# Kernel optimization log

Measured on AMD Instinct MI355X. Metric: run time of the kernel, lower is better.

Reference implementation:

```python
import jax, jax.numpy as jnp
import numpy as np

NUM_HEADS = 12


def setup_inputs() -> dict:
    key = jax.random.key(0)
    k_x, k_m, k_qkv, k_proj = jax.random.split(key, 4)
    B, N, C = 2, 2048, 768
    x = jax.random.normal(k_x, (B, N, C), dtype=jnp.float32)
    # binary key mask: 1 = attend, 0 = masked out
    mask = jax.random.randint(k_m, (B, N), 0, 2).astype(jnp.int32)
    # torch Linear(dim, dim*3, bias=False): stored here as [in, out]
    w_qkv = jax.random.normal(k_qkv, (C, 3 * C), dtype=jnp.float32) * 0.02
    w_proj = jax.random.normal(k_proj, (C, C), dtype=jnp.float32) * 0.02
    b_proj = jnp.zeros((C,), dtype=jnp.float32)
    return {"x": x, "mask": mask, "w_qkv": w_qkv, "w_proj": w_proj, "b_proj": b_proj}


def reference(x, mask, w_qkv, w_proj, b_proj):
    B, N, C = x.shape
    H = NUM_HEADS
    hd = C // H
    scale = hd ** -0.5
    qkv = (x @ w_qkv).reshape(B, N, 3, H, hd)
    q, k, v = jnp.moveaxis(qkv, 2, 0)            # each [B, N, H, hd]
    attn = jnp.einsum('bnhd,bmhd->bhnm', q, k) * scale  # [B, H, N, N]
    # faithful masked_softmax: unstable exp (no max subtraction), mask keys, renormalize
    m = mask.astype(x.dtype)[:, None, None, :]   # [B, 1, 1, N]
    x_exp = jnp.exp(attn) * m
    attn = x_exp / x_exp.sum(-1, keepdims=True)
    out = jnp.einsum('bhnm,bmhd->bnhd', attn, v).reshape(B, N, C)
    return out @ w_proj + b_proj
```

## Files before the change

kernel.cpp:

```cpp
#include <hip/hip_runtime.h>
#include <cstdint>

#define NB 2
#define NSEQ 2048
#define CDIM 768
#define NH 12
#define HD 64
#define NTOK (NB*NSEQ)
#define QKV_COLS (3*CDIM)
#define NBLK ((NSEQ/64)*NH*NB)

typedef short bf16x8 __attribute__((ext_vector_type(8)));
typedef short bf16x4 __attribute__((ext_vector_type(4)));
typedef float f32x4  __attribute__((ext_vector_type(4)));
typedef short short4v __attribute__((ext_vector_type(4)));
typedef unsigned int uint4v __attribute__((ext_vector_type(4)));

#define MFMA16(a,b,c) __builtin_amdgcn_mfma_f32_16x16x32_bf16(a,b,c,0,0,0)

__device__ __forceinline__ short f2b(float f) {
    uint32_t u = __builtin_bit_cast(uint32_t, f);
    u += 0x7fffu + ((u >> 16) & 1u);
    return (short)(u >> 16);
}
__device__ __forceinline__ float b2f(short s) {
    return __builtin_bit_cast(float, (uint32_t)((uint32_t)(unsigned short)s << 16));
}
__device__ __forceinline__ unsigned pack2(float a, float b) {
    unsigned ua = __builtin_bit_cast(unsigned, a) + 0x7fffu;
    unsigned ub = __builtin_bit_cast(unsigned, b) + 0x7fffu;
    return __builtin_amdgcn_perm(ub, ua, 0x07060302u);
}
__device__ __forceinline__ float fexp2(float x) {
#if __has_builtin(__builtin_amdgcn_exp2f)
    return __builtin_amdgcn_exp2f(x);
#else
    return __expf(x * 0.69314718055994531f);
#endif
}
__device__ __forceinline__ void gll16(const short* g, short* l) {
    __builtin_amdgcn_global_load_lds(
        (const __attribute__((address_space(1))) unsigned int*)g,
        (__attribute__((address_space(3))) unsigned int*)l, 16, 0, 0);
}

__global__ __launch_bounds__(256) void prep_kernel(
    const float* __restrict__ x, const float* __restrict__ w_qkv,
    const float* __restrict__ w_proj, const int* __restrict__ mask,
    short* __restrict__ xb, short* __restrict__ wqt, short* __restrict__ wpt,
    short* __restrict__ maskb)
{
    __shared__ float tile[32][33];
    const int bid = blockIdx.x, t = threadIdx.x;
    if (bid < 3072) {
        int i = bid * 256 + t;
        float4 v = ((const float4*)x)[i];
        short4v o = { f2b(v.x), f2b(v.y), f2b(v.z), f2b(v.w) };
        ((short4v*)xb)[i] = o;
        return;
    }
    if (bid >= 5376) {
        int i = ((bid - 5376) << 11) + (t << 3);
        int4 a = *(const int4*)(mask + i);
        int4 c = *(const int4*)(mask + i + 4);
        const short NEG = (short)0xC680;
        short4v o0 = { a.x ? (short)0 : NEG, a.y ? (short)0 : NEG,
                       a.z ? (short)0 : NEG, a.w ? (short)0 : NEG };
        short4v o1 = { c.x ? (short)0 : NEG, c.y ? (short)0 : NEG,
                       c.z ? (short)0 : NEG, c.w ? (short)0 : NEG };
        *(short4v*)(maskb + i) = o0;
        *(short4v*)(maskb + i + 4) = o1;
        return;
    }
    const float* w; short* wt; int K, NC, n0, k0;
    if (bid < 3072 + 1728) {
        int r = bid - 3072;
        w = w_qkv; wt = wqt; K = CDIM; NC = QKV_COLS;
        n0 = (r % 72) * 32; k0 = (r / 72) * 32;
    } else {
        int r = bid - 4800;
        w = w_proj; wt = wpt; K = CDIM; NC = CDIM;
        n0 = (r % 24) * 32; k0 = (r / 24) * 32;
    }
    #pragma unroll
    for (int i = 0; i < 4; ++i) {
        int idx = t + i * 256; int r = idx >> 5, c = idx & 31;
        tile[r][c] = w[(size_t)(k0 + r) * NC + n0 + c];
    }
    __syncthreads();
    #pragma unroll
    for (int i = 0; i < 4; ++i) {
        int idx = t + i * 256; int r = idx >> 5, c = idx & 31;
        wt[(size_t)(n0 + r) * K + k0 + c] = f2b(tile[c][r]);
    }
}

__global__ __launch_bounds__(256) void gemm_qkv(
    const short* __restrict__ A ,
    const short* __restrict__ B ,
    short* __restrict__ qb, short* __restrict__ kb, short* __restrict__ vt)
{
    __shared__ short As[128 * 32];
    __shared__ short Bs[128 * 32];
    const int t = threadIdx.x;
    const int lane = t & 63, wid = t >> 6;
    const int quad = lane >> 4, l16 = lane & 15;
    const int wA = wid >> 1, wB = wid & 1;
    const int n0 = blockIdx.x * 128;
    const int m0 = blockIdx.y * 128;

    const int srow = wid * 16 + (lane >> 2), schunk = (lane & 3) * 8;
    const short* ag0 = A + (size_t)(n0 + srow) * CDIM + schunk;
    const short* ag1 = ag0 + (size_t)64 * CDIM;
    const short* bg0 = B + (size_t)(m0 + srow) * CDIM + schunk;
    const short* bg1 = bg0 + (size_t)64 * CDIM;
    short* asl0 = &As[(wid * 16) * 32];
    short* asl1 = &As[(wid * 16 + 64) * 32];
    short* bsl0 = &Bs[(wid * 16) * 32];
    short* bsl1 = &Bs[(wid * 16 + 64) * 32];

    f32x4 acc[4][4] = {};
    for (int k0 = 0; k0 < CDIM; k0 += 32) {
        __syncthreads();
        gll16(ag0 + k0, asl0);
        gll16(ag1 + k0, asl1);
        gll16(bg0 + k0, bsl0);
        gll16(bg1 + k0, bsl1);
        __syncthreads();
        bf16x8 af[4], bf[4];
        #pragma unroll
        for (int i = 0; i < 4; ++i)
            af[i] = *(const bf16x8*)&As[(wA*64 + i*16 + l16) * 32 + quad*8];
        #pragma unroll
        for (int j = 0; j < 4; ++j)
            bf[j] = *(const bf16x8*)&Bs[(wB*64 + j*16 + l16) * 32 + quad*8];
        #pragma unroll
        for (int i = 0; i < 4; ++i)
            #pragma unroll
            for (int j = 0; j < 4; ++j)
                acc[i][j] = MFMA16(af[i], bf[j], acc[i][j]);
    }

    const int colbase = n0 + wA * 64;
    const int s = colbase / CDIM;
    const int h = (colbase - s * CDIM) >> 6;
    const int b = m0 >> 11;
    const size_t bh = (size_t)(b * NH + h);
    const float qsc = (s == 0) ? 0.18033688011112042f : 1.0f;
    #pragma unroll
    for (int i = 0; i < 4; ++i) {
        const int d0 = i*16 + quad*4;
        #pragma unroll
        for (int j = 0; j < 4; ++j) {
            int tok = (m0 + wB*64 + j*16 + l16) & (NSEQ - 1);
            if (s < 2) {
                short* dst = (s == 0 ? qb : kb) + (bh * NSEQ + tok) * HD + d0;
                short4v o = { f2b(acc[i][j][0] * qsc), f2b(acc[i][j][1] * qsc),
                              f2b(acc[i][j][2] * qsc), f2b(acc[i][j][3] * qsc) };
                *(short4v*)dst = o;
            } else {
                short* dst = vt + (bh * HD + d0) * NSEQ + tok;
                #pragma unroll
                for (int r = 0; r < 4; ++r)
                    dst[(size_t)r * NSEQ] = f2b(acc[i][j][r]);
            }
        }
    }
}

#define STAGE_K(KT, BUF) do {                                                    \
    short* kb_ = (BUF);                                                          \
    _Pragma("unroll")                                                            \
    for (int j = 0; j < 4; ++j)                                                  \
        gll16(kp + (size_t)((KT) + rK[j]) * HD + cK[j]*8,                        \
              kb_ + wid*2048 + j*512);                                           \
} while (0)

#define STAGE_V(KT) do {                                                         \
    _Pragma("unroll")                                                            \
    for (int j = 0; j < 4; ++j)                                                  \
        gll16(vp + (size_t)dV[j] * NSEQ + (KT) + cV[j]*8,                        \
              Vb + wid*2048 + j*512);                                            \
} while (0)

#define QKBODY(KT, KBUF) do {                                                    \
    const short* KsB_ = (KBUF) + kg*4096;                                        \
    _Pragma("unroll")                                                            \
    for (int ks = 0; ks < 2; ++ks) {                                             \
        short4v mi0_ = *(const short4v*)&Msk[(KT) + kg*64 + ks*16 + qrow4];      \
        short4v mi1_ = *(const short4v*)&Msk[(KT) + kg*64 + 32 + ks*16 + qrow4]; \
        const int kro_ = (ks*16 + l16) * 64;                                     \
        bf16x8 kf00_ = *(const bf16x8*)&KsB_[kro_ + kc0];                        \
        bf16x8 kf01_ = *(const bf16x8*)&KsB_[kro_ + kc1];                        \
        bf16x8 kf10_ = *(const bf16x8*)&KsB_[2048 + kro_ + kc0];                 \
        bf16x8 kf11_ = *(const bf16x8*)&KsB_[2048 + kro_ + kc1];                 \
        f32x4 m0v_ = { b2f(mi0_[0]), b2f(mi0_[1]),                               \
                       b2f(mi0_[2]), b2f(mi0_[3]) };                             \
        f32x4 m1v_ = { b2f(mi1_[0]), b2f(mi1_[1]),                               \
                       b2f(mi1_[2]), b2f(mi1_[3]) };                             \
        _Pragma("unroll")                                                        \
        for (int jq = 0; jq < 2; ++jq) {                                         \
            f32x4 s0_ = m0v_, s1_ = m1v_;                                        \
            s0_ = MFMA16(kf00_, qf[jq][0], s0_);                                 \
            s0_ = MFMA16(kf01_, qf[jq][1], s0_);                                 \
            s1_ = MFMA16(kf10_, qf[jq][0], s1_);                                 \
            s1_ = MFMA16(kf11_, qf[jq][1], s1_);                                 \
            float e0 = fexp2(s0_[0]);                                            \
            float e1 = fexp2(s0_[1]);                                            \
            float e2 = fexp2(s0_[2]);                                            \
            float e3 = fexp2(s0_[3]);                                            \
            float f0 = fexp2(s1_[0]);                                            \
            float f1 = fexp2(s1_[1]);                                            \
            float f2 = fexp2(s1_[2]);                                            \
            float f3 = fexp2(s1_[3]);                                            \
            uint4v pk_ = { pack2(e0, e1), pack2(e2, e3),                         \
                           pack2(f0, f1), pack2(f2, f3) };                       \
            pb[jq][ks] = __builtin_bit_cast(bf16x8, pk_);                        \
        }                                                                        \
    }                                                                            \
} while (0)

#define PVBODY() do {                                                            \
    _Pragma("unroll")                                                            \
    for (int ks = 0; ks < 2; ++ks) {                                             \
        lacc[0] = MFMA16(onesv, pb[0][ks], lacc[0]);                             \
        lacc[1] = MFMA16(onesv, pb[1][ks], lacc[1]);                             \
    }                                                                            \
    _Pragma("unroll")                                                            \
    for (int it = 0; it < 4; ++it) {                                             \
        const int vrow_ = (it*16 + l16) * 128;                                   \
        _Pragma("unroll")                                                        \
        for (int ks = 0; ks < 2; ++ks) {                                         \
            const int gl_ = (((kg*8 + ks*2 + qh) ^ l16) << 3) + vsub;            \
            const int gh_ = (((kg*8 + 4 + ks*2 + qh) ^ l16) << 3) + vsub;        \
            bf16x4 lo_ = *(const bf16x4*)&Vb[vrow_ + gl_];                       \
            bf16x4 hi_ = *(const bf16x4*)&Vb[vrow_ + gh_];                       \
            bf16x8 vf_ = __builtin_shufflevector(lo_, hi_, 0,1,2,3,4,5,6,7);     \
            o_acc[0][it] = MFMA16(vf_, pb[0][ks], o_acc[0][it]);                 \
            o_acc[1][it] = MFMA16(vf_, pb[1][ks], o_acc[1][it]);                 \
        }                                                                        \
    }                                                                            \
} while (0)

#define WAITV_BAR() do {                                                         \
    asm volatile("s_waitcnt vmcnt(4)" ::: "memory");                             \
    __builtin_amdgcn_sched_barrier(0);                                           \
    __builtin_amdgcn_s_barrier();                                                \
} while (0)

#define WAITK_BAR() do {                                                         \
    asm volatile("s_waitcnt vmcnt(0)" ::: "memory");                             \
    __builtin_amdgcn_sched_barrier(0);                                           \
    __builtin_amdgcn_s_barrier();                                                \
} while (0)

__global__ __launch_bounds__(256, 3) void attn_kernel(
    const short* __restrict__ qb, const short* __restrict__ kb,
    const short* __restrict__ vt, const short* __restrict__ maskb,
    short* __restrict__ ao)
{
    __shared__ __align__(16) short Kb[2][8192];
    __shared__ __align__(16) short Vb[8192];
    __shared__ __align__(16) short Msk[2048];

    const int t = threadIdx.x;
    const int lane = t & 63, wid = t >> 6;
    const int quad = lane >> 4, l16 = lane & 15;
    const int qg = wid >> 1, kg = wid & 1;
    const int id = blockIdx.x;
    const int idx = id >> 3;
    const int bh = (id & 7) + ((idx % 3) << 3);
    const int q0 = (idx / 3) << 6;
    const int b = bh / NH, h = bh - b * NH;
    const size_t hoff = (size_t)bh * NSEQ * HD;
    const short* qp = qb + hoff;
    const short* kp = kb + hoff;
    const short* vp = vt + hoff;
    const int qrow4 = quad * 4;

    int rK[4], cK[4], dV[4], cV[4];
    #pragma unroll
    for (int j = 0; j < 4; ++j) {
        int o = wid * 4096 + j * 1024 + lane * 16;
        rK[j] = o >> 7;
        cK[j] = ((o >> 4) & 7) ^ (rK[j] & 7);
        dV[j] = o >> 8;
        cV[j] = ((o >> 4) & 15) ^ (dV[j] & 15);
    }
    const int r7 = l16 & 7;
    const int kc0 = ((quad     ^ r7) << 3);
    const int kc1 = (((quad+4) ^ r7) << 3);
    const int qh = quad >> 1;
    const int vsub = (quad & 1) * 4;

    bf16x8 qf[2][2];
    {
        const short* qr = qp + (size_t)(q0 + qg*32 + l16) * HD + quad*8;
        qf[0][0] = *(const bf16x8*)qr;
        qf[0][1] = *(const bf16x8*)(qr + 32);
        qf[1][0] = *(const bf16x8*)(qr + 16*HD);
        qf[1][1] = *(const bf16x8*)(qr + 16*HD + 32);
    }

    const short one_ = (short)0x3F80;
    const bf16x8 onesv = { one_, one_, one_, one_, one_, one_, one_, one_ };

    f32x4 o_acc[2][4] = {};
    f32x4 lacc[2] = {};
    bf16x8 pb[2][2];

    STAGE_K(0, Kb[0]);
    gll16(maskb + b * NSEQ + t * 8, Msk + wid * 512);
    __syncthreads();

    for (int kt = 0; kt < NSEQ; kt += 256) {
        STAGE_V(kt);
        __builtin_amdgcn_sched_barrier(0);
        STAGE_K(kt + 128, Kb[1]);
        __builtin_amdgcn_sched_barrier(0);
        QKBODY(kt, Kb[0]);
        WAITV_BAR();
        __builtin_amdgcn_s_setprio(1);
        PVBODY();
        __builtin_amdgcn_s_setprio(0);
        WAITK_BAR();

        STAGE_V(kt + 128);
        __builtin_amdgcn_sched_barrier(0);
        STAGE_K((kt + 256) & (NSEQ - 1), Kb[0]);
        __builtin_amdgcn_sched_barrier(0);
        QKBODY(kt + 128, Kb[1]);
        WAITV_BAR();
        __builtin_amdgcn_s_setprio(1);
        PVBODY();
        __builtin_amdgcn_s_setprio(0);
        WAITK_BAR();
    }

    f32x4* red = (f32x4*)Kb;
    const int rbase = (qg*64 + lane) * 9;
    if (kg == 1) {
        #pragma unroll
        for (int jq = 0; jq < 2; ++jq)
            #pragma unroll
            for (int it = 0; it < 4; ++it)
                red[rbase + jq*4 + it] = o_acc[jq][it];
        f32x4 lv = { lacc[0][0], lacc[1][0], 0.f, 0.f };
        red[rbase + 8] = lv;
    }
    __syncthreads();
    if (kg == 0) {
        f32x4 lv = red[rbase + 8];
        const float inv0 = 1.0f / (lacc[0][0] + lv[0]);
        const float inv1 = 1.0f / (lacc[1][0] + lv[1]);
        #pragma unroll
        for (int jq = 0; jq < 2; ++jq) {
            const float inv = jq ? inv1 : inv0;
            const int tok = b * NSEQ + q0 + qg*32 + jq*16 + l16;
            short* dst = ao + (size_t)tok * CDIM + h * HD + qrow4;
            #pragma unroll
            for (int it = 0; it < 4; ++it) {
                f32x4 o_ = o_acc[jq][it];
                f32x4 r_ = red[rbase + jq*4 + it];
                short4v o = { f2b((o_[0] + r_[0]) * inv),
                              f2b((o_[1] + r_[1]) * inv),
                              f2b((o_[2] + r_[2]) * inv),
                              f2b((o_[3] + r_[3]) * inv) };
                *(short4v*)(dst + it*16) = o;
            }
        }
    }
}

__global__ __launch_bounds__(256) void gemm_proj(
    const short* __restrict__ A ,
    const short* __restrict__ B ,
    const float* __restrict__ bias, float* __restrict__ out)
{
    __shared__ short As[128 * 32];
    __shared__ short Bs[128 * 32];
    const int t = threadIdx.x;
    const int lane = t & 63, wid = t >> 6;
    const int quad = lane >> 4, l16 = lane & 15;
    const int wA = wid >> 1, wB = wid & 1;
    const int n0 = blockIdx.x * 128;
    const int m0 = blockIdx.y * 128;

    const int srow = wid * 16 + (lane >> 2), schunk = (lane & 3) * 8;
    const short* ag0 = A + (size_t)(n0 + srow) * CDIM + schunk;
    const short* ag1 = ag0 + (size_t)64 * CDIM;
    const short* bg0 = B + (size_t)(m0 + srow) * CDIM + schunk;
    const short* bg1 = bg0 + (size_t)64 * CDIM;
    short* asl0 = &As[(wid * 16) * 32];
    short* asl1 = &As[(wid * 16 + 64) * 32];
    short* bsl0 = &Bs[(wid * 16) * 32];
    short* bsl1 = &Bs[(wid * 16 + 64) * 32];

    f32x4 acc[4][4] = {};
    for (int k0 = 0; k0 < CDIM; k0 += 32) {
        __syncthreads();
        gll16(ag0 + k0, asl0);
        gll16(ag1 + k0, asl1);
        gll16(bg0 + k0, bsl0);
        gll16(bg1 + k0, bsl1);
        __syncthreads();
        bf16x8 af[4], bf[4];
        #pragma unroll
        for (int i = 0; i < 4; ++i)
            af[i] = *(const bf16x8*)&As[(wA*64 + i*16 + l16) * 32 + quad*8];
        #pragma unroll
        for (int j = 0; j < 4; ++j)
            bf[j] = *(const bf16x8*)&Bs[(wB*64 + j*16 + l16) * 32 + quad*8];
        #pragma unroll
        for (int i = 0; i < 4; ++i)
            #pragma unroll
            for (int j = 0; j < 4; ++j)
                acc[i][j] = MFMA16(af[i], bf[j], acc[i][j]);
    }

    #pragma unroll
    for (int i = 0; i < 4; ++i) {
        int col0 = n0 + wA*64 + i*16 + quad*4;
        float4 bias4 = *(const float4*)&bias[col0];
        #pragma unroll
        for (int j = 0; j < 4; ++j) {
            int tok = m0 + wB*64 + j*16 + l16;
            float4 o = { acc[i][j][0] + bias4.x, acc[i][j][1] + bias4.y,
                         acc[i][j][2] + bias4.z, acc[i][j][3] + bias4.w };
            *(float4*)(out + (size_t)tok * CDIM + col0) = o;
        }
    }
}

extern "C" void kernel_launch(void* const* d_in, const int* in_sizes, int n_in,
                              void* d_out, int out_size, void* d_ws, size_t ws_size,
                              hipStream_t stream)
{
    const float* x      = (const float*)d_in[0];
    const int*   mask   = (const int*)d_in[1];
    const float* w_qkv  = (const float*)d_in[2];
    const float* w_proj = (const float*)d_in[3];
    const float* b_proj = (const float*)d_in[4];
    float* out = (float*)d_out;

    const size_t SZ = (size_t)NTOK * CDIM;
    short* xb  = (short*)d_ws;
    short* wqt = xb  + SZ;
    short* wpt = wqt + (size_t)QKV_COLS * CDIM;
    short* qb  = wpt + (size_t)CDIM * CDIM;
    short* kb  = qb  + SZ;
    short* vt  = kb  + SZ;
    short* ao  = vt  + SZ;
    short* maskb = ao + SZ;

    dim3 blk(256);
    prep_kernel<<<dim3(5378), blk, 0, stream>>>(x, w_qkv, w_proj, mask,
                                                xb, wqt, wpt, maskb);
    gemm_qkv<<<dim3(QKV_COLS/128, NTOK/128), blk, 0, stream>>>(wqt, xb, qb, kb, vt);
    attn_kernel<<<dim3(NBLK), blk, 0, stream>>>(qb, kb, vt, maskb, ao);
    gemm_proj<<<dim3(CDIM/128, NTOK/128), blk, 0, stream>>>(wpt, ao, b_proj, out);
}
```

Baseline: 159.0 us.

## Double-buffer LDS tiles in QKV and projection GEMMs; vectorize weight transpose

Both GEMM kernels now keep two LDS stages: the next K-tile is loaded with direct global-to-LDS loads while MFMAs run on the current one, and there is one barrier per iteration instead of two. The aim is to hide global load latency behind the matrix math. The weight transpose/convert prep kernel now reads float4 and writes short4 per thread instead of scalar loops. LDS use per block doubles, which may lower occupancy. Whether the async LDS writes are ordered correctly depends on the barrier also waiting on the outstanding loads.

```diff
diff --git a/kernel.cpp b/kernel.cpp
--- a/kernel.cpp
+++ b/kernel.cpp
@@ -82,26 +82,34 @@
         w = w_proj; wt = wpt; K = CDIM; NC = CDIM;
         n0 = (r % 24) * 32; k0 = (r / 24) * 32;
     }
-    #pragma unroll
-    for (int i = 0; i < 4; ++i) {
-        int idx = t + i * 256; int r = idx >> 5, c = idx & 31;
-        tile[r][c] = w[(size_t)(k0 + r) * NC + n0 + c];
+    const int r = t >> 3, c4 = (t & 7) * 4;
+    {
+        float4 v = *(const float4*)&w[(size_t)(k0 + r) * NC + n0 + c4];
+        tile[r][c4 + 0] = v.x; tile[r][c4 + 1] = v.y;
+        tile[r][c4 + 2] = v.z; tile[r][c4 + 3] = v.w;
     }
     __syncthreads();
-    #pragma unroll
-    for (int i = 0; i < 4; ++i) {
-        int idx = t + i * 256; int r = idx >> 5, c = idx & 31;
-        wt[(size_t)(n0 + r) * K + k0 + c] = f2b(tile[c][r]);
-    }
-}
+    {
+        short4v o = { f2b(tile[c4 + 0][r]), f2b(tile[c4 + 1][r]),
+                      f2b(tile[c4 + 2][r]), f2b(tile[c4 + 3][r]) };
+        *(short4v*)&wt[(size_t)(n0 + r) * K + k0 + c4] = o;
+    }
+}
+
+#define GSTAGE(K0V, B) do {                                                      \
+    gll16(ag0 + (K0V), As + (B)*4096 + (wid*16)*32);                             \
+    gll16(ag1 + (K0V), As + (B)*4096 + (wid*16 + 64)*32);                        \
+    gll16(bg0 + (K0V), Bs + (B)*4096 + (wid*16)*32);                             \
+    gll16(bg1 + (K0V), Bs + (B)*4096 + (wid*16 + 64)*32);                        \
+} while (0)
 
 __global__ __launch_bounds__(256) void gemm_qkv(
     const short* __restrict__ A ,
     const short* __restrict__ B ,
     short* __restrict__ qb, short* __restrict__ kb, short* __restrict__ vt)
 {
-    __shared__ short As[128 * 32];
-    __shared__ short Bs[128 * 32];
+    __shared__ short As[2 * 4096];
+    __shared__ short Bs[2 * 4096];
     const int t = threadIdx.x;
     const int lane = t & 63, wid = t >> 6;
     const int quad = lane >> 4, l16 = lane & 15;
@@ -114,31 +122,30 @@
     const short* ag1 = ag0 + (size_t)64 * CDIM;
     const short* bg0 = B + (size_t)(m0 + srow) * CDIM + schunk;
     const short* bg1 = bg0 + (size_t)64 * CDIM;
-    short* asl0 = &As[(wid * 16) * 32];
-    short* asl1 = &As[(wid * 16 + 64) * 32];
-    short* bsl0 = &Bs[(wid * 16) * 32];
-    short* bsl1 = &Bs[(wid * 16 + 64) * 32];
 
     f32x4 acc[4][4] = {};
+    GSTAGE(0, 0);
+    __syncthreads();
+    int buf = 0;
     for (int k0 = 0; k0 < CDIM; k0 += 32) {
-        __syncthreads();
-        gll16(ag0 + k0, asl0);
-        gll16(ag1 + k0, asl1);
-        gll16(bg0 + k0, bsl0);
-        gll16(bg1 + k0, bsl1);
-        __syncthreads();
+        if (k0 + 32 < CDIM) GSTAGE(k0 + 32, buf ^ 1);
+        __builtin_amdgcn_sched_barrier(0);
+        const short* As_ = As + buf * 4096;
+        const short* Bs_ = Bs + buf * 4096;
         bf16x8 af[4], bf[4];
         #pragma unroll
         for (int i = 0; i < 4; ++i)
-            af[i] = *(const bf16x8*)&As[(wA*64 + i*16 + l16) * 32 + quad*8];
+            af[i] = *(const bf16x8*)&As_[(wA*64 + i*16 + l16) * 32 + quad*8];
         #pragma unroll
         for (int j = 0; j < 4; ++j)
-            bf[j] = *(const bf16x8*)&Bs[(wB*64 + j*16 + l16) * 32 + quad*8];
+            bf[j] = *(const bf16x8*)&Bs_[(wB*64 + j*16 + l16) * 32 + quad*8];
         #pragma unroll
         for (int i = 0; i < 4; ++i)
             #pragma unroll
             for (int j = 0; j < 4; ++j)
                 acc[i][j] = MFMA16(af[i], bf[j], acc[i][j]);
+        __syncthreads();
+        buf ^= 1;
     }
 
     const int colbase = n0 + wA * 64;
@@ -377,8 +384,8 @@
     const short* __restrict__ B ,
     const float* __restrict__ bias, float* __restrict__ out)
 {
-    __shared__ short As[128 * 32];
-    __shared__ short Bs[128 * 32];
+    __shared__ short As[2 * 4096];
+    __shared__ short Bs[2 * 4096];
     const int t = threadIdx.x;
     const int lane = t & 63, wid = t >> 6;
     const int quad = lane >> 4, l16 = lane & 15;
@@ -391,31 +398,30 @@
     const short* ag1 = ag0 + (size_t)64 * CDIM;
     const short* bg0 = B + (size_t)(m0 + srow) * CDIM + schunk;
     const short* bg1 = bg0 + (size_t)64 * CDIM;
-    short* asl0 = &As[(wid * 16) * 32];
-    short* asl1 = &As[(wid * 16 + 64) * 32];
-    short* bsl0 = &Bs[(wid * 16) * 32];
-    short* bsl1 = &Bs[(wid * 16 + 64) * 32];
 
     f32x4 acc[4][4] = {};
+    GSTAGE(0, 0);
+    __syncthreads();
+    int buf = 0;
     for (int k0 = 0; k0 < CDIM; k0 += 32) {
-        __syncthreads();
-        gll16(ag0 + k0, asl0);
-        gll16(ag1 + k0, asl1);
-        gll16(bg0 + k0, bsl0);
-        gll16(bg1 + k0, bsl1);
-        __syncthreads();
+        if (k0 + 32 < CDIM) GSTAGE(k0 + 32, buf ^ 1);
+        __builtin_amdgcn_sched_barrier(0);
+        const short* As_ = As + buf * 4096;
+        const short* Bs_ = Bs + buf * 4096;
         bf16x8 af[4], bf[4];
         #pragma unroll
         for (int i = 0; i < 4; ++i)
-            af[i] = *(const bf16x8*)&As[(wA*64 + i*16 + l16) * 32 + quad*8];
+            af[i] = *(const bf16x8*)&As_[(wA*64 + i*16 + l16) * 32 + quad*8];
         #pragma unroll
         for (int j = 0; j < 4; ++j)
-            bf[j] = *(const bf16x8*)&Bs[(wB*64 + j*16 + l16) * 32 + quad*8];
+            bf[j] = *(const bf16x8*)&Bs_[(wB*64 + j*16 + l16) * 32 + quad*8];
         #pragma unroll
         for (int i = 0; i < 4; ++i)
             #pragma unroll
             for (int j = 0; j < 4; ++j)
                 acc[i][j] = MFMA16(af[i], bf[j], acc[i][j]);
+        __syncthreads();
+        buf ^= 1;
     }
 
     #pragma unroll
```

New measurement: 158.6 us. No clear change (-0.2%).
